# Kernel optimization log

Hardware: AMD Instinct MI355X
Metric: run time of the kernel (lower is better)

Reference implementation:

```python
import jax, jax.numpy as jnp
import numpy as np

B = 262144
I = 128   # input_len
H = 128   # h_len (must equal c_len structurally)
C = 128   # c_len
O = 128   # output_len
STD = 0.05  # keras random_normal default stddev


def setup_inputs() -> dict:
    key = jax.random.key(0)
    ks = jax.random.split(key, 14)
    inp = {
        "c_": jax.random.normal(ks[0], (B, C), dtype=jnp.float32),
        "h_": jax.random.normal(ks[1], (B, H), dtype=jnp.float32),
        "x": jax.random.normal(ks[2], (B, I), dtype=jnp.float32),
        # gate weights [C, I+H] and biases [C]
        "w": jax.random.normal(ks[3], (C, I + H), dtype=jnp.float32) * STD,
        "wi": jax.random.normal(ks[4], (C, I + H), dtype=jnp.float32) * STD,
        "wf": jax.random.normal(ks[5], (C, I + H), dtype=jnp.float32) * STD,
        "wo": jax.random.normal(ks[6], (C, I + H), dtype=jnp.float32) * STD,
        "w_out": jax.random.normal(ks[7], (O, H), dtype=jnp.float32) * STD,
        "b": jax.random.normal(ks[8], (C,), dtype=jnp.float32) * STD,
        "bi": jax.random.normal(ks[9], (C,), dtype=jnp.float32) * STD,
        "bf": jax.random.normal(ks[10], (C,), dtype=jnp.float32) * STD,
        "bo": jax.random.normal(ks[11], (C,), dtype=jnp.float32) * STD,
        "b_out": jax.random.normal(ks[12], (O,), dtype=jnp.float32) * STD,
    }
    return inp


def reference(c_, h_, x, w, wi, wf, wo, w_out, b, bi, bf, bo, b_out):
    # [B, I+H]
    xh = jnp.concatenate([x, h_], axis=-1)
    # Fuse the 4 gate matmuls into one GEMM with stacked weights [4C, I+H]
    W = jnp.concatenate([w, wi, wf, wo], axis=0)
    Bv = jnp.concatenate([b, bi, bf, bo], axis=0)
    gates = xh @ W.T + Bv                      # [B, 4C]
    gz, gi, gf, go = jnp.split(gates, 4, axis=-1)
    z = jnp.tanh(gz)
    zi = jax.nn.sigmoid(gi)
    zf = jax.nn.sigmoid(gf)
    zo = jax.nn.sigmoid(go)
    c = zf * c_ + zi * z                       # [B, C]
    h = zo * jnp.tanh(c)                       # [B, C] (== H)
    y = jax.nn.sigmoid(h @ w_out.T + b_out)    # [B, O]
    return (c, h, y)
```

## Files before the change

kernel.cpp:

```cpp
#include <hip/hip_runtime.h>

#define TB 262144

typedef short bf16x8 __attribute__((ext_vector_type(8)));
typedef float f32x16 __attribute__((ext_vector_type(16)));
typedef float f32x4v __attribute__((ext_vector_type(4)));

__device__ __forceinline__ unsigned short f2bf(float f) {
  unsigned int u = __float_as_uint(f);
  unsigned int r = (u + 0x7fffu + ((u >> 16) & 1u)) >> 16;
  return (unsigned short)r;
}
__device__ __forceinline__ float sigmoid_f(float x) {
  return __builtin_amdgcn_rcpf(1.f + __expf(-x));
}
__device__ __forceinline__ float tanh_f(float x) {
  return 1.f - 2.f * __builtin_amdgcn_rcpf(__expf(2.f * x) + 1.f);
}

#define LDS_BARRIER() asm volatile("s_waitcnt lgkmcnt(0)\n\ts_barrier" ::: "memory")

__global__ void wconv_kernel(const float* __restrict__ w, const float* __restrict__ wi,
                             const float* __restrict__ wf, const float* __restrict__ wo,
                             const float* __restrict__ wout, unsigned short* __restrict__ dst) {
  int i = blockIdx.x * 256 + threadIdx.x;
  float v;
  if (i < 32768) v = w[i];
  else if (i < 65536) v = wi[i - 32768];
  else if (i < 98304) v = wf[i - 65536];
  else if (i < 131072) v = wo[i - 98304];
  else v = wout[i - 131072];
  dst[i] = f2bf(v);
}

__global__ __launch_bounds__(256, 4) void lstm_main(
    const float* __restrict__ c_prev, const float* __restrict__ h_prev,
    const float* __restrict__ x, const unsigned short* __restrict__ wbf,
    const float* __restrict__ b, const float* __restrict__ bi,
    const float* __restrict__ bf_, const float* __restrict__ bo,
    const float* __restrict__ b_out,
    float* __restrict__ out_c, float* __restrict__ out_h, float* __restrict__ out_y) {
  __shared__ unsigned short us_xh[8192];
  __shared__ unsigned short us_h[4096];

  const int tid = threadIdx.x;
  const int wave = tid >> 6;
  const int lane = tid & 63;
  const int l31 = lane & 31;
  const int lhi = lane >> 5;
  const int kb_lane = lhi * 8;
  const int row0 = blockIdx.x * 32;
  const int jcol = wave * 32 + l31;

  {
#pragma unroll
    for (int it = 0; it < 4; ++it) {
      const int cid = it * 256 + tid;
      const int r = cid >> 5;
      const int c4 = (cid & 31) * 4;
      const f32x4v vx = __builtin_nontemporal_load(
          reinterpret_cast<const f32x4v*>(&x[(size_t)(row0 + r) * 128 + c4]));
      ushort4 ux; ux.x = f2bf(vx.x); ux.y = f2bf(vx.y); ux.z = f2bf(vx.z); ux.w = f2bf(vx.w);
      *reinterpret_cast<ushort4*>(&us_xh[(r * 256 + c4) ^ ((r & 7) << 3)]) = ux;
    }
#pragma unroll
    for (int it = 0; it < 4; ++it) {
      const int cid = it * 256 + tid;
      const int r = cid >> 5;
      const int c4 = (cid & 31) * 4;
      const f32x4v vh = __builtin_nontemporal_load(
          reinterpret_cast<const f32x4v*>(&h_prev[(size_t)(row0 + r) * 128 + c4]));
      ushort4 uh; uh.x = f2bf(vh.x); uh.y = f2bf(vh.y); uh.z = f2bf(vh.z); uh.w = f2bf(vh.w);
      *reinterpret_cast<ushort4*>(&us_xh[(r * 256 + 128 + c4) ^ ((r & 7) << 3)]) = uh;
    }
  }
  LDS_BARRIER();

  float cpre[16];
#pragma unroll
  for (int reg = 0; reg < 16; ++reg) {
    const int r = (reg & 3) + 8 * (reg >> 2) + 4 * lhi;
    cpre[reg] = __builtin_nontemporal_load(&c_prev[(size_t)(row0 + r) * 128 + jcol]);
  }
  const float bz_s = b[jcol];
  const float bi_s = bi[jcol];
  const float bf_s = bf_[jcol];
  const float bo_s = bo[jcol];

  f32x16 accz = {}, acci = {}, accf = {}, acco = {};
#pragma unroll
  for (int kk = 0; kk < 16; ++kk) {
    const int kb = kk * 16 + kb_lane;
    const bf16x8 a8 =
        *reinterpret_cast<const bf16x8*>(&us_xh[(l31 * 256 + kb) ^ ((l31 & 7) << 3)]);
    const int woff = jcol * 256 + kb;
    const bf16x8 bz8 = *reinterpret_cast<const bf16x8*>(&wbf[woff]);
    const bf16x8 bi8 = *reinterpret_cast<const bf16x8*>(&wbf[32768 + woff]);
    const bf16x8 bf8 = *reinterpret_cast<const bf16x8*>(&wbf[65536 + woff]);
    const bf16x8 bo8 = *reinterpret_cast<const bf16x8*>(&wbf[98304 + woff]);
    accz = __builtin_amdgcn_mfma_f32_32x32x16_bf16(a8, bz8, accz, 0, 0, 0);
    acci = __builtin_amdgcn_mfma_f32_32x32x16_bf16(a8, bi8, acci, 0, 0, 0);
    accf = __builtin_amdgcn_mfma_f32_32x32x16_bf16(a8, bf8, accf, 0, 0, 0);
    acco = __builtin_amdgcn_mfma_f32_32x32x16_bf16(a8, bo8, acco, 0, 0, 0);
  }

#pragma unroll
  for (int reg = 0; reg < 16; ++reg) {
    const int r = (reg & 3) + 8 * (reg >> 2) + 4 * lhi;
    const size_t gi = (size_t)(row0 + r) * 128 + jcol;
    const float z  = tanh_f(accz[reg] + bz_s);
    const float zi = sigmoid_f(acci[reg] + bi_s);
    const float zf = sigmoid_f(accf[reg] + bf_s);
    const float zo = sigmoid_f(acco[reg] + bo_s);
    const float cvv = zf * cpre[reg] + zi * z;
    const float hvv = zo * tanh_f(cvv);
    __builtin_nontemporal_store(cvv, &out_c[gi]);
    __builtin_nontemporal_store(hvv, &out_h[gi]);
    us_h[(r * 128 + jcol) ^ ((r & 7) << 3)] = f2bf(hvv);
  }
  LDS_BARRIER();

  f32x16 accy = {};
#pragma unroll
  for (int ks = 0; ks < 8; ++ks) {
    const int kb = ks * 16 + kb_lane;
    const bf16x8 a8 =
        *reinterpret_cast<const bf16x8*>(&us_h[(l31 * 128 + kb) ^ ((l31 & 7) << 3)]);
    const bf16x8 bw =
        *reinterpret_cast<const bf16x8*>(&wbf[131072 + jcol * 128 + kb]);
    accy = __builtin_amdgcn_mfma_f32_32x32x16_bf16(a8, bw, accy, 0, 0, 0);
  }
  const float by_s = b_out[jcol];
#pragma unroll
  for (int reg = 0; reg < 16; ++reg) {
    const int r = (reg & 3) + 8 * (reg >> 2) + 4 * lhi;
    __builtin_nontemporal_store(sigmoid_f(accy[reg] + by_s),
                                &out_y[(size_t)(row0 + r) * 128 + jcol]);
  }
}

extern "C" void kernel_launch(void* const* d_in, const int* in_sizes, int n_in,
                              void* d_out, int out_size, void* d_ws, size_t ws_size,
                              hipStream_t stream) {
  const float* c_    = (const float*)d_in[0];
  const float* h_    = (const float*)d_in[1];
  const float* x     = (const float*)d_in[2];
  const float* w     = (const float*)d_in[3];
  const float* wi    = (const float*)d_in[4];
  const float* wf    = (const float*)d_in[5];
  const float* wo    = (const float*)d_in[6];
  const float* wout  = (const float*)d_in[7];
  const float* b     = (const float*)d_in[8];
  const float* bi    = (const float*)d_in[9];
  const float* bf_   = (const float*)d_in[10];
  const float* bo    = (const float*)d_in[11];
  const float* b_out = (const float*)d_in[12];

  unsigned short* wbf = (unsigned short*)d_ws;
  float* out_c = (float*)d_out;
  float* out_h = out_c + (size_t)TB * 128;
  float* out_y = out_h + (size_t)TB * 128;

  hipLaunchKernelGGL(wconv_kernel, dim3(576), dim3(256), 0, stream,
                     w, wi, wf, wo, wout, wbf);
  hipLaunchKernelGGL(lstm_main, dim3(8192), dim3(256), 0, stream,
                     c_, h_, x, wbf, b, bi, bf_, bo, b_out, out_c, out_h, out_y);
}
```

Measured before the change: 377.7 us.

## Restructure LSTM kernel to 16-row tiles with per-gate waves and LDS gate exchange

Switches from 32x32x16 MFMA with 4 waves each computing all four gates for 32 columns to 16x16x32 MFMA with 8 waves, where each wave pair owns one gate. Activated gates are staged through LDS in bf16 so the elementwise LSTM update runs with vectorized float4 loads and stores of c and h. Block size grows to 512 threads over 16 rows, with twice as many blocks. The aim is more parallelism and coalesced elementwise I/O. In exchange it adds an extra barrier and LDS round trip, halves how many rows reuse each weight load, rounds gate activations to bf16 before the cell update, and leaves half the waves idle in the output GEMM.

```diff
diff --git a/kernel.cpp b/kernel.cpp
--- a/kernel.cpp
+++ b/kernel.cpp
@@ -3,13 +3,16 @@
 #define TB 262144
 
 typedef short bf16x8 __attribute__((ext_vector_type(8)));
-typedef float f32x16 __attribute__((ext_vector_type(16)));
 typedef float f32x4v __attribute__((ext_vector_type(4)));
+typedef unsigned short u16x4 __attribute__((ext_vector_type(4)));
 
 __device__ __forceinline__ unsigned short f2bf(float f) {
   unsigned int u = __float_as_uint(f);
   unsigned int r = (u + 0x7fffu + ((u >> 16) & 1u)) >> 16;
   return (unsigned short)r;
+}
+__device__ __forceinline__ float bf2f(unsigned short u) {
+  return __uint_as_float(((unsigned int)u) << 16);
 }
 __device__ __forceinline__ float sigmoid_f(float x) {
   return __builtin_amdgcn_rcpf(1.f + __expf(-x));
@@ -33,109 +36,129 @@
   dst[i] = f2bf(v);
 }
 
-__global__ __launch_bounds__(256, 4) void lstm_main(
+__global__ __launch_bounds__(512, 6) void lstm_main(
     const float* __restrict__ c_prev, const float* __restrict__ h_prev,
     const float* __restrict__ x, const unsigned short* __restrict__ wbf,
     const float* __restrict__ b, const float* __restrict__ bi,
     const float* __restrict__ bf_, const float* __restrict__ bo,
     const float* __restrict__ b_out,
     float* __restrict__ out_c, float* __restrict__ out_h, float* __restrict__ out_y) {
-  __shared__ unsigned short us_xh[8192];
-  __shared__ unsigned short us_h[4096];
+  __shared__ unsigned short smem[14592];
+  unsigned short* us_xh = smem;
+  unsigned short* gts   = smem + 4096;
+  unsigned short* us_h  = smem + 12544;
 
   const int tid = threadIdx.x;
   const int wave = tid >> 6;
   const int lane = tid & 63;
-  const int l31 = lane & 31;
-  const int lhi = lane >> 5;
-  const int kb_lane = lhi * 8;
-  const int row0 = blockIdx.x * 32;
-  const int jcol = wave * 32 + l31;
+  const int lr = lane & 15;
+  const int lq = lane >> 4;
+  const int row0 = blockIdx.x * 16;
 
   {
+    const int t8 = tid & 255;
+    const int r = t8 >> 4;
+    const int k8 = (t8 & 15) * 8;
+    const float* src = (tid < 256) ? &x[(size_t)(row0 + r) * 128 + k8]
+                                   : &h_prev[(size_t)(row0 + r) * 128 + k8];
+    const f32x4v v0 = __builtin_nontemporal_load(reinterpret_cast<const f32x4v*>(src));
+    const f32x4v v1 = __builtin_nontemporal_load(reinterpret_cast<const f32x4v*>(src + 4));
+    const int kb = k8 + ((tid < 256) ? 0 : 128);
+    const int idx = (r * 256 + kb) ^ ((r & 7) << 3);
+    u16x4 u0, u1;
+    u0[0] = f2bf(v0[0]); u0[1] = f2bf(v0[1]); u0[2] = f2bf(v0[2]); u0[3] = f2bf(v0[3]);
+    u1[0] = f2bf(v1[0]); u1[1] = f2bf(v1[1]); u1[2] = f2bf(v1[2]); u1[3] = f2bf(v1[3]);
+    *reinterpret_cast<u16x4*>(&us_xh[idx]) = u0;
+    *reinterpret_cast<u16x4*>(&us_xh[idx + 4]) = u1;
+  }
+  const int erow = tid >> 5;
+  const int ec4 = (tid & 31) * 4;
+  const f32x4v cpre = __builtin_nontemporal_load(
+      reinterpret_cast<const f32x4v*>(&c_prev[(size_t)(row0 + erow) * 128 + ec4]));
+
+  LDS_BARRIER();
+
+  const int g = wave >> 1;
+  const int colbase = (wave & 1) * 64;
+  const unsigned short* wg = wbf + g * 32768;
+  f32x4v acc[4] = {};
 #pragma unroll
-    for (int it = 0; it < 4; ++it) {
-      const int cid = it * 256 + tid;
-      const int r = cid >> 5;
-      const int c4 = (cid & 31) * 4;
-      const f32x4v vx = __builtin_nontemporal_load(
-          reinterpret_cast<const f32x4v*>(&x[(size_t)(row0 + r) * 128 + c4]));
-      ushort4 ux; ux.x = f2bf(vx.x); ux.y = f2bf(vx.y); ux.z = f2bf(vx.z); ux.w = f2bf(vx.w);
-      *reinterpret_cast<ushort4*>(&us_xh[(r * 256 + c4) ^ ((r & 7) << 3)]) = ux;
+  for (int kk = 0; kk < 8; ++kk) {
+    const int aidx = (lr * 256 + kk * 32 + lq * 8) ^ ((lr & 7) << 3);
+    const bf16x8 a8 = *reinterpret_cast<const bf16x8*>(&us_xh[aidx]);
+#pragma unroll
+    for (int cf = 0; cf < 4; ++cf) {
+      const int col = colbase + cf * 16 + lr;
+      const bf16x8 wf8 =
+          *reinterpret_cast<const bf16x8*>(&wg[col * 256 + kk * 32 + lq * 8]);
+      acc[cf] = __builtin_amdgcn_mfma_f32_16x16x32_bf16(a8, wf8, acc[cf], 0, 0, 0);
     }
+  }
+
+  const float* bp = (g == 0) ? b : (g == 1) ? bi : (g == 2) ? bf_ : bo;
 #pragma unroll
-    for (int it = 0; it < 4; ++it) {
-      const int cid = it * 256 + tid;
-      const int r = cid >> 5;
-      const int c4 = (cid & 31) * 4;
-      const f32x4v vh = __builtin_nontemporal_load(
-          reinterpret_cast<const f32x4v*>(&h_prev[(size_t)(row0 + r) * 128 + c4]));
-      ushort4 uh; uh.x = f2bf(vh.x); uh.y = f2bf(vh.y); uh.z = f2bf(vh.z); uh.w = f2bf(vh.w);
-      *reinterpret_cast<ushort4*>(&us_xh[(r * 256 + 128 + c4) ^ ((r & 7) << 3)]) = uh;
+  for (int cf = 0; cf < 4; ++cf) {
+    const int col = colbase + cf * 16 + lr;
+    const float bias = bp[col];
+#pragma unroll
+    for (int ri = 0; ri < 4; ++ri) {
+      const int rrow = lq * 4 + ri;
+      float v = acc[cf][ri] + bias;
+      v = (g == 0) ? tanh_f(v) : sigmoid_f(v);
+      gts[g * 2112 + rrow * 132 + col] = f2bf(v);
     }
   }
   LDS_BARRIER();
 
-  float cpre[16];
+  {
+    const u16x4 uz = *reinterpret_cast<const u16x4*>(&gts[0 * 2112 + erow * 132 + ec4]);
+    const u16x4 ui = *reinterpret_cast<const u16x4*>(&gts[1 * 2112 + erow * 132 + ec4]);
+    const u16x4 uf = *reinterpret_cast<const u16x4*>(&gts[2 * 2112 + erow * 132 + ec4]);
+    const u16x4 uo = *reinterpret_cast<const u16x4*>(&gts[3 * 2112 + erow * 132 + ec4]);
+    f32x4v cv, hv;
+    u16x4 hb;
 #pragma unroll
-  for (int reg = 0; reg < 16; ++reg) {
-    const int r = (reg & 3) + 8 * (reg >> 2) + 4 * lhi;
-    cpre[reg] = __builtin_nontemporal_load(&c_prev[(size_t)(row0 + r) * 128 + jcol]);
-  }
-  const float bz_s = b[jcol];
-  const float bi_s = bi[jcol];
-  const float bf_s = bf_[jcol];
-  const float bo_s = bo[jcol];
-
-  f32x16 accz = {}, acci = {}, accf = {}, acco = {};
-#pragma unroll
-  for (int kk = 0; kk < 16; ++kk) {
-    const int kb = kk * 16 + kb_lane;
-    const bf16x8 a8 =
-        *reinterpret_cast<const bf16x8*>(&us_xh[(l31 * 256 + kb) ^ ((l31 & 7) << 3)]);
-    const int woff = jcol * 256 + kb;
-    const bf16x8 bz8 = *reinterpret_cast<const bf16x8*>(&wbf[woff]);
-    const bf16x8 bi8 = *reinterpret_cast<const bf16x8*>(&wbf[32768 + woff]);
-    const bf16x8 bf8 = *reinterpret_cast<const bf16x8*>(&wbf[65536 + woff]);
-    const bf16x8 bo8 = *reinterpret_cast<const bf16x8*>(&wbf[98304 + woff]);
-    accz = __builtin_amdgcn_mfma_f32_32x32x16_bf16(a8, bz8, accz, 0, 0, 0);
-    acci = __builtin_amdgcn_mfma_f32_32x32x16_bf16(a8, bi8, acci, 0, 0, 0);
-    accf = __builtin_amdgcn_mfma_f32_32x32x16_bf16(a8, bf8, accf, 0, 0, 0);
-    acco = __builtin_amdgcn_mfma_f32_32x32x16_bf16(a8, bo8, acco, 0, 0, 0);
-  }
-
-#pragma unroll
-  for (int reg = 0; reg < 16; ++reg) {
-    const int r = (reg & 3) + 8 * (reg >> 2) + 4 * lhi;
-    const size_t gi = (size_t)(row0 + r) * 128 + jcol;
-    const float z  = tanh_f(accz[reg] + bz_s);
-    const float zi = sigmoid_f(acci[reg] + bi_s);
-    const float zf = sigmoid_f(accf[reg] + bf_s);
-    const float zo = sigmoid_f(acco[reg] + bo_s);
-    const float cvv = zf * cpre[reg] + zi * z;
-    const float hvv = zo * tanh_f(cvv);
-    __builtin_nontemporal_store(cvv, &out_c[gi]);
-    __builtin_nontemporal_store(hvv, &out_h[gi]);
-    us_h[(r * 128 + jcol) ^ ((r & 7) << 3)] = f2bf(hvv);
+    for (int j = 0; j < 4; ++j) {
+      const float z  = bf2f(uz[j]);
+      const float zi = bf2f(ui[j]);
+      const float zf = bf2f(uf[j]);
+      const float zo = bf2f(uo[j]);
+      const float c = zf * cpre[j] + zi * z;
+      const float h = zo * tanh_f(c);
+      cv[j] = c;
+      hv[j] = h;
+      hb[j] = f2bf(h);
+    }
+    const size_t gi = (size_t)(row0 + erow) * 128 + ec4;
+    __builtin_nontemporal_store(cv, reinterpret_cast<f32x4v*>(&out_c[gi]));
+    __builtin_nontemporal_store(hv, reinterpret_cast<f32x4v*>(&out_h[gi]));
+    *reinterpret_cast<u16x4*>(&us_h[(erow * 128 + ec4) ^ ((erow & 7) << 3)]) = hb;
   }
   LDS_BARRIER();
 
-  f32x16 accy = {};
+  if (wave < 4) {
+    f32x4v acc2[2] = {};
 #pragma unroll
-  for (int ks = 0; ks < 8; ++ks) {
-    const int kb = ks * 16 + kb_lane;
-    const bf16x8 a8 =
-        *reinterpret_cast<const bf16x8*>(&us_h[(l31 * 128 + kb) ^ ((l31 & 7) << 3)]);
-    const bf16x8 bw =
-        *reinterpret_cast<const bf16x8*>(&wbf[131072 + jcol * 128 + kb]);
-    accy = __builtin_amdgcn_mfma_f32_32x32x16_bf16(a8, bw, accy, 0, 0, 0);
-  }
-  const float by_s = b_out[jcol];
+    for (int ks = 0; ks < 4; ++ks) {
+      const int aidx = (lr * 128 + ks * 32 + lq * 8) ^ ((lr & 7) << 3);
+      const bf16x8 a8 = *reinterpret_cast<const bf16x8*>(&us_h[aidx]);
 #pragma unroll
-  for (int reg = 0; reg < 16; ++reg) {
-    const int r = (reg & 3) + 8 * (reg >> 2) + 4 * lhi;
-    __builtin_nontemporal_store(sigmoid_f(accy[reg] + by_s),
-                                &out_y[(size_t)(row0 + r) * 128 + jcol]);
+      for (int cf = 0; cf < 2; ++cf) {
+        const int col = wave * 32 + cf * 16 + lr;
+        const bf16x8 w2 =
+            *reinterpret_cast<const bf16x8*>(&wbf[131072 + col * 128 + ks * 32 + lq * 8]);
+        acc2[cf] = __builtin_amdgcn_mfma_f32_16x16x32_bf16(a8, w2, acc2[cf], 0, 0, 0);
+      }
+    }
+#pragma unroll
+    for (int ri = 0; ri < 4; ++ri) {
+      const int rrow = lq * 4 + ri;
+      const size_t gr = (size_t)(row0 + rrow) * 128;
+      const int col0 = wave * 32 + lr;
+      const int col1 = col0 + 16;
+      __builtin_nontemporal_store(sigmoid_f(acc2[0][ri] + b_out[col0]), &out_y[gr + col0]);
+      __builtin_nontemporal_store(sigmoid_f(acc2[1][ri] + b_out[col1]), &out_y[gr + col1]);
+    }
   }
 }
 
@@ -163,6 +186,6 @@
 
   hipLaunchKernelGGL(wconv_kernel, dim3(576), dim3(256), 0, stream,
                      w, wi, wf, wo, wout, wbf);
-  hipLaunchKernelGGL(lstm_main, dim3(8192), dim3(256), 0, stream,
+  hipLaunchKernelGGL(lstm_main, dim3(16384), dim3(512), 0, stream,
                      c_, h_, x, wbf, b, bi, bf_, bo, b_out, out_c, out_h, out_y);
 }
```

After: 592.8 us. 1.57x slower.
